# Kernel optimization log

Measured on AMD Instinct MI355X. Metric: run time of the kernel, lower is better.

Reference implementation:

```python
import jax, jax.numpy as jnp
import numpy as np

D_MODEL = 1024
N_HEADS = 16
D_HEAD = D_MODEL // N_HEADS
SCALE = 1.0 / np.sqrt(D_HEAD)


def setup_inputs() -> dict:
    key = jax.random.key(0)
    ks = jax.random.split(key, 5)
    B, S = 2, 2048
    x = jax.random.normal(ks[0], (B, S, D_MODEL), dtype=jnp.float32)
    # torch F.linear weights have shape (d_out, d_in); kaiming-uniform-ish init
    bound = 1.0 / np.sqrt(D_MODEL)
    Wq = jax.random.uniform(ks[1], (D_MODEL, D_MODEL), jnp.float32, -bound, bound)
    Wk = jax.random.uniform(ks[2], (D_MODEL, D_MODEL), jnp.float32, -bound, bound)
    Wv = jax.random.uniform(ks[3], (D_MODEL, D_MODEL), jnp.float32, -bound, bound)
    Wo = jax.random.uniform(ks[4], (D_MODEL, D_MODEL), jnp.float32, -bound, bound)
    return {"x": x, "Wq": Wq, "Wk": Wk, "Wv": Wv, "Wo": Wo}


def reference(x, Wq, Wk, Wv, Wo):
    B, S, _ = x.shape
    # F.linear(x, W) = x @ W.T; reshape to [B, H, S, Dh]
    def proj(W):
        return (x @ W.T).reshape(B, S, N_HEADS, D_HEAD).transpose(0, 2, 1, 3)
    Q, K, V = proj(Wq), proj(Wk), proj(Wv)
    # scores [B, H, S, S]
    attn = jnp.einsum('bhqd,bhkd->bhqk', Q, K) * SCALE
    causal = jnp.tril(jnp.ones((S, S), dtype=bool))
    attn = jnp.where(causal, attn, -jnp.inf)
    attn = jax.nn.softmax(attn, axis=-1)
    out = jnp.einsum('bhqk,bhkd->bhqd', attn, V)
    out = out.transpose(0, 2, 1, 3).reshape(B, S, D_MODEL)
    return out @ Wo.T
```

## Files before the change

### kernel.cpp

```cpp
#include <hip/hip_runtime.h>


typedef __attribute__((ext_vector_type(8))) short short8;
typedef __attribute__((ext_vector_type(4))) float f32x4;
typedef __attribute__((ext_vector_type(4))) _Float16 half4;

#if __has_builtin(__builtin_amdgcn_exp2f)
#define EXP2F(x) __builtin_amdgcn_exp2f(x)
#else
#define EXP2F(x) exp2f(x)
#endif

__device__ __forceinline__ unsigned short f2bf(float f) {
  unsigned int x = __float_as_uint(f);
  x += 0x7fffu + ((x >> 16) & 1u);
  return (unsigned short)(x >> 16);
}

__device__ __forceinline__ void gload16(const void* g, void* l) {
  __builtin_amdgcn_global_load_lds(
      (const __attribute__((address_space(1))) void*)g,
      (__attribute__((address_space(3))) void*)l, 16, 0, 0);
}

__device__ __forceinline__ int swz64(int row, int sc) {
  return row * 64 + ((((sc >> 3) ^ (row & 7)) << 3) | (sc & 7));
}

__device__ __forceinline__ int swzG(int row, int chunk) {
  return row * 32 + (((chunk ^ ((row >> 1) & 3)) << 3));
}

__global__ void cast_kernel(const float* __restrict__ x, const float* __restrict__ wq,
                            const float* __restrict__ wk, const float* __restrict__ wv,
                            const float* __restrict__ wo,
                            unsigned short* __restrict__ xb, unsigned short* __restrict__ wqb,
                            unsigned short* __restrict__ wkb, unsigned short* __restrict__ wvb,
                            unsigned short* __restrict__ wob) {
  int id = blockIdx.x;
  const float* in; unsigned short* out; int blk; float sc = 1.f;
  if (id < 4096) { in = x; out = xb; blk = id; }
  else {
    int wsel = (id - 4096) >> 10;
    blk = (id - 4096) & 1023;
    switch (wsel) {
      case 0: in = wq; out = wqb; sc = 0.18033688011112042f; break;
      case 1: in = wk; out = wkb; break;
      case 2: in = wv; out = wvb; break;
      default: in = wo; out = wob; break;
    }
  }
  int i = blk * 256 + threadIdx.x;
  float4 v = ((const float4*)in)[i];
  union { unsigned short u[4]; uint2 p; } o;
  o.u[0] = f2bf(v.x * sc); o.u[1] = f2bf(v.y * sc);
  o.u[2] = f2bf(v.z * sc); o.u[3] = f2bf(v.w * sc);
  ((uint2*)out)[i] = o.p;
}

#define GK 1024

__global__ __launch_bounds__(256) void gemm_qkv_kernel(
    const unsigned short* __restrict__ X,
    const unsigned short* __restrict__ Wq,
    const unsigned short* __restrict__ Wk,
    const unsigned short* __restrict__ Wv,
    unsigned short* __restrict__ Qo,
    unsigned short* __restrict__ Ko,
    _Float16* __restrict__ Vt) {
  __shared__ unsigned short As[2][128 * 32];
  __shared__ unsigned short Bs[2][128 * 32];
  int mb = blockIdx.x;
  int nbT = blockIdx.y;
  int sel = nbT >> 3, nb = nbT & 7;
  const unsigned short* W = sel == 0 ? Wq : (sel == 1 ? Wk : Wv);

  int tid = threadIdx.x;
  int w = tid >> 6, l = tid & 63, quad = l >> 4, lo = l & 15;
  int wm = (w >> 1) * 64, wn = (w & 1) * 64;

  int srow = tid >> 2;
  int slc = (tid & 3) ^ ((srow >> 1) & 3);
  int srow2 = (256 + tid) >> 2;
  int slc2 = (tid & 3) ^ ((srow2 >> 1) & 3);

  f32x4 acc[4][4];
#pragma unroll
  for (int i = 0; i < 4; i++)
#pragma unroll
    for (int j = 0; j < 4; j++) acc[i][j] = (f32x4){0.f, 0.f, 0.f, 0.f};

  gload16(X + (size_t)(mb * 128 + srow) * GK + slc * 8, (char*)As[0] + tid * 16);
  gload16(W + (size_t)(nb * 128 + srow) * GK + slc * 8, (char*)Bs[0] + tid * 16);
  gload16(X + (size_t)(mb * 128 + srow2) * GK + slc2 * 8, (char*)As[0] + (256 + tid) * 16);
  gload16(W + (size_t)(nb * 128 + srow2) * GK + slc2 * 8, (char*)Bs[0] + (256 + tid) * 16);

  for (int kt = 0; kt < 32; kt++) {
    __syncthreads();
    if (kt + 1 < 32) {
      int nb_ = (kt + 1) & 1, k0 = (kt + 1) * 32;
      gload16(X + (size_t)(mb * 128 + srow) * GK + k0 + slc * 8, (char*)As[nb_] + tid * 16);
      gload16(W + (size_t)(nb * 128 + srow) * GK + k0 + slc * 8, (char*)Bs[nb_] + tid * 16);
      gload16(X + (size_t)(mb * 128 + srow2) * GK + k0 + slc2 * 8,
              (char*)As[nb_] + (256 + tid) * 16);
      gload16(W + (size_t)(nb * 128 + srow2) * GK + k0 + slc2 * 8,
              (char*)Bs[nb_] + (256 + tid) * 16);
    }
    const unsigned short* as = As[kt & 1];
    const unsigned short* bs = Bs[kt & 1];
    short8 a[4], b[4];
#pragma unroll
    for (int mi = 0; mi < 4; mi++)
      a[mi] = *(const short8*)&as[swzG(wm + mi * 16 + lo, quad)];
#pragma unroll
    for (int ni = 0; ni < 4; ni++)
      b[ni] = *(const short8*)&bs[swzG(wn + ni * 16 + lo, quad)];
#pragma unroll
    for (int mi = 0; mi < 4; mi++)
#pragma unroll
      for (int ni = 0; ni < 4; ni++)
        acc[mi][ni] = __builtin_amdgcn_mfma_f32_16x16x32_bf16(a[mi], b[ni],
                                                              acc[mi][ni], 0, 0, 0);
  }
  if (sel == 2) {
#pragma unroll
    for (int mi = 0; mi < 4; mi++)
#pragma unroll
      for (int ni = 0; ni < 4; ni++) {
        int row0 = mb * 128 + wm + mi * 16 + quad * 4;
        int col = nb * 128 + wn + ni * 16 + lo;
        int bb = row0 >> 11, ss = row0 & 2047;
        int hh = col >> 6, dd = col & 63;
        half4 v;
#pragma unroll
        for (int r = 0; r < 4; r++) v[r] = (_Float16)acc[mi][ni][r];
        *(half4*)&Vt[((size_t)((bb * 16 + hh) * 64 + dd)) * 2048 + ss] = v;
      }
  } else {
    unsigned short* C = sel == 0 ? Qo : Ko;
#pragma unroll
    for (int mi = 0; mi < 4; mi++)
#pragma unroll
      for (int ni = 0; ni < 4; ni++)
#pragma unroll
        for (int r = 0; r < 4; r++) {
          int row = mb * 128 + wm + mi * 16 + quad * 4 + r;
          int col = nb * 128 + wn + ni * 16 + lo;
          C[(size_t)row * 1024 + col] = f2bf(acc[mi][ni][r]);
        }
  }
}

__global__ __launch_bounds__(256) void gemm_out_kernel(
    const unsigned short* __restrict__ A,
    const unsigned short* __restrict__ W,
    float* __restrict__ C) {
  __shared__ unsigned short As[2][128 * 32];
  __shared__ unsigned short Bs[2][64 * 32];
  int mb = blockIdx.x, nb = blockIdx.y;
  int tid = threadIdx.x;
  int w = tid >> 6, l = tid & 63, quad = l >> 4, lo = l & 15;
  int wm = w * 32;

  int srow = tid >> 2;
  int slc = (tid & 3) ^ ((srow >> 1) & 3);
  int srow2 = (256 + tid) >> 2;
  int slc2 = (tid & 3) ^ ((srow2 >> 1) & 3);

  f32x4 acc[2][4];
#pragma unroll
  for (int i = 0; i < 2; i++)
#pragma unroll
    for (int j = 0; j < 4; j++) acc[i][j] = (f32x4){0.f, 0.f, 0.f, 0.f};

  gload16(A + (size_t)(mb * 128 + srow) * GK + slc * 8, (char*)As[0] + tid * 16);
  gload16(A + (size_t)(mb * 128 + srow2) * GK + slc2 * 8, (char*)As[0] + (256 + tid) * 16);
  gload16(W + (size_t)(nb * 64 + srow) * GK + slc * 8, (char*)Bs[0] + tid * 16);

  for (int kt = 0; kt < 32; kt++) {
    __syncthreads();
    if (kt + 1 < 32) {
      int nb_ = (kt + 1) & 1, k0 = (kt + 1) * 32;
      gload16(A + (size_t)(mb * 128 + srow) * GK + k0 + slc * 8, (char*)As[nb_] + tid * 16);
      gload16(A + (size_t)(mb * 128 + srow2) * GK + k0 + slc2 * 8,
              (char*)As[nb_] + (256 + tid) * 16);
      gload16(W + (size_t)(nb * 64 + srow) * GK + k0 + slc * 8, (char*)Bs[nb_] + tid * 16);
    }
    const unsigned short* as = As[kt & 1];
    const unsigned short* bs = Bs[kt & 1];
    short8 a[2], b[4];
#pragma unroll
    for (int mi = 0; mi < 2; mi++)
      a[mi] = *(const short8*)&as[swzG(wm + mi * 16 + lo, quad)];
#pragma unroll
    for (int ni = 0; ni < 4; ni++)
      b[ni] = *(const short8*)&bs[swzG(ni * 16 + lo, quad)];
#pragma unroll
    for (int mi = 0; mi < 2; mi++)
#pragma unroll
      for (int ni = 0; ni < 4; ni++)
        acc[mi][ni] = __builtin_amdgcn_mfma_f32_16x16x32_bf16(a[mi], b[ni],
                                                              acc[mi][ni], 0, 0, 0);
  }
#pragma unroll
  for (int mi = 0; mi < 2; mi++)
#pragma unroll
    for (int ni = 0; ni < 4; ni++)
#pragma unroll
      for (int r = 0; r < 4; r++) {
        int row = mb * 128 + wm + mi * 16 + quad * 4 + r;
        int col = nb * 64 + ni * 16 + lo;
        C[(size_t)row * 1024 + col] = acc[mi][ni][r];
      }
}

__global__ __launch_bounds__(256, 4) void attn_kernel(
    const unsigned short* __restrict__ Q,
    const unsigned short* __restrict__ K,
    const _Float16* __restrict__ Vt,
    unsigned short* __restrict__ O) {
  const int S = 2048, DM = 1024;
  __shared__ unsigned short Ks[2][64 * 64];
  __shared__ _Float16 Vts[2][64 * 64];

  int id = blockIdx.x;
  int bh = id & 31;
  int qt = 31 - (id >> 5);
  int b = bh >> 4, h = bh & 15;
  size_t base = (size_t)b * S * DM + h * 64;
  size_t baseVt = (size_t)(bh * 64) * S;

  int tid = threadIdx.x;
  int w = tid >> 6, lane = tid & 63, quad = lane >> 4, lo = lane & 15;
  int qrow0 = qt * 64 + w * 16;
  const half4 ones = {(_Float16)1.f, (_Float16)1.f, (_Float16)1.f, (_Float16)1.f};

  short8 qf[2];
#pragma unroll
  for (int d = 0; d < 2; d++)
    qf[d] = *(const short8*)(Q + base + (size_t)(qrow0 + lo) * DM + d * 32 + quad * 8);

#pragma unroll
  for (int j = 0; j < 2; j++) {
    int s_ = j * 256 + tid;
    int row = s_ >> 3, lc = (s_ & 7) ^ (row & 7);
    gload16(K + base + (size_t)row * DM + lc * 8, (char*)Ks[0] + s_ * 16);
    gload16(Vt + baseVt + (size_t)row * S + lc * 8, (char*)Vts[0] + s_ * 16);
  }

  f32x4 oacc[4], lacc;
  lacc = (f32x4){0.f, 0.f, 0.f, 0.f};
#pragma unroll
  for (int ni = 0; ni < 4; ni++) oacc[ni] = (f32x4){0.f, 0.f, 0.f, 0.f};

  int tend = qt + 1;
  for (int t = 0; t < tend; t++) {
    __syncthreads();
    if (t + 1 < tend) {
      int tb = (t + 1) & 1;
#pragma unroll
      for (int j = 0; j < 2; j++) {
        int s_ = j * 256 + tid;
        int row = s_ >> 3, lc = (s_ & 7) ^ (row & 7);
        gload16(K + base + (size_t)((t + 1) * 64 + row) * DM + lc * 8,
                (char*)Ks[tb] + s_ * 16);
        gload16(Vt + baseVt + (size_t)row * S + (t + 1) * 64 + lc * 8,
                (char*)Vts[tb] + s_ * 16);
      }
    }
    const unsigned short* ks = Ks[t & 1];
    const _Float16* vs = Vts[t & 1];

    f32x4 st[4];
#pragma unroll
    for (int kvt = 0; kvt < 4; kvt++) st[kvt] = (f32x4){0.f, 0.f, 0.f, 0.f};
#pragma unroll
    for (int kvt = 0; kvt < 4; kvt++)
#pragma unroll
      for (int d = 0; d < 2; d++) {
        short8 kf = *(const short8*)&ks[swz64(kvt * 16 + lo, d * 32 + quad * 8)];
        st[kvt] = __builtin_amdgcn_mfma_f32_16x16x32_bf16(kf, qf[d], st[kvt], 0, 0, 0);
      }

    if (t == tend - 1) {
      int qg = qrow0 + lo;
#pragma unroll
      for (int kvt = 0; kvt < 4; kvt++)
#pragma unroll
        for (int r = 0; r < 4; r++) {
          int kv = t * 64 + kvt * 16 + quad * 4 + r;
          if (kv > qg) st[kvt][r] = -1e30f;
        }
    }

    half4 pf[4];
#pragma unroll
    for (int kvt = 0; kvt < 4; kvt++) {
      half4 p4;
#pragma unroll
      for (int r = 0; r < 4; r++) p4[r] = (_Float16)EXP2F(st[kvt][r]);
      pf[kvt] = p4;
    }

#pragma unroll
    for (int kvt = 0; kvt < 4; kvt++) {
#pragma unroll
      for (int ni = 0; ni < 4; ni++) {
        half4 vf = *(const half4*)&vs[swz64(ni * 16 + lo, kvt * 16 + quad * 4)];
        oacc[ni] = __builtin_amdgcn_mfma_f32_16x16x16f16(pf[kvt], vf, oacc[ni], 0, 0, 0);
      }
      lacc = __builtin_amdgcn_mfma_f32_16x16x16f16(pf[kvt], ones, lacc, 0, 0, 0);
    }
  }

  float inv[4];
#pragma unroll
  for (int r = 0; r < 4; r++) inv[r] = 1.0f / lacc[r];
#pragma unroll
  for (int ni = 0; ni < 4; ni++)
#pragma unroll
    for (int r = 0; r < 4; r++) {
      int qg = qrow0 + quad * 4 + r;
      O[base + (size_t)qg * DM + ni * 16 + lo] = f2bf(oacc[ni][r] * inv[r]);
    }
}

extern "C" void kernel_launch(void* const* d_in, const int* in_sizes, int n_in,
                              void* d_out, int out_size, void* d_ws, size_t ws_size,
                              hipStream_t stream) {
  const float* x  = (const float*)d_in[0];
  const float* Wq = (const float*)d_in[1];
  const float* Wk = (const float*)d_in[2];
  const float* Wv = (const float*)d_in[3];
  const float* Wo = (const float*)d_in[4];
  float* out = (float*)d_out;
  char* ws = (char*)d_ws;

  unsigned short* Xb  = (unsigned short*)(ws);
  unsigned short* Wqb = (unsigned short*)(ws + (8ll  << 20));
  unsigned short* Wkb = (unsigned short*)(ws + (10ll << 20));
  unsigned short* Wvb = (unsigned short*)(ws + (12ll << 20));
  unsigned short* Wob = (unsigned short*)(ws + (14ll << 20));
  unsigned short* Qb  = (unsigned short*)(ws + (16ll << 20));
  unsigned short* Kb  = (unsigned short*)(ws + (24ll << 20));
  _Float16*       Vt  = (_Float16*)     (ws + (32ll << 20));
  unsigned short* Ob  = (unsigned short*)(ws + (40ll << 20));

  cast_kernel<<<8192, 256, 0, stream>>>(x, Wq, Wk, Wv, Wo, Xb, Wqb, Wkb, Wvb, Wob);
  gemm_qkv_kernel<<<dim3(32, 24), 256, 0, stream>>>(Xb, Wqb, Wkb, Wvb, Qb, Kb, Vt);
  attn_kernel<<<1024, 256, 0, stream>>>(Qb, Kb, Vt, Ob);
  gemm_out_kernel<<<dim3(32, 16), 256, 0, stream>>>(Ob, Wob, out);
}
```

Measured before the change: 178.4 us.

## Triple-buffer GEMM LDS tiles with two-stage-ahead async prefetch

Both projection GEMM kernels move from double to triple LDS buffering. Global-to-LDS loads are issued two k-tiles ahead, and the loop uses explicit s_waitcnt vmcnt plus a raw s_barrier in place of __syncthreads, so only the oldest tile's loads must finish before compute. This aims to hide more global memory latency. The cost is about 50% more shared memory per block, which may lower occupancy, and correctness now depends on the hand-counted vmcnt values.

```diff
diff --git a/kernel.cpp b/kernel.cpp
--- a/kernel.cpp
+++ b/kernel.cpp
@@ -68,8 +68,8 @@
     unsigned short* __restrict__ Qo,
     unsigned short* __restrict__ Ko,
     _Float16* __restrict__ Vt) {
-  __shared__ unsigned short As[2][128 * 32];
-  __shared__ unsigned short Bs[2][128 * 32];
+  __shared__ unsigned short As[3][128 * 32];
+  __shared__ unsigned short Bs[3][128 * 32];
   int mb = blockIdx.x;
   int nbT = blockIdx.y;
   int sel = nbT >> 3, nb = nbT & 7;
@@ -84,30 +84,42 @@
   int srow2 = (256 + tid) >> 2;
   int slc2 = (tid & 3) ^ ((srow2 >> 1) & 3);
 
+  const unsigned short* Xa = X + (size_t)(mb * 128 + srow) * GK + slc * 8;
+  const unsigned short* Wa = W + (size_t)(nb * 128 + srow) * GK + slc * 8;
+  const unsigned short* Xa2 = X + (size_t)(mb * 128 + srow2) * GK + slc2 * 8;
+  const unsigned short* Wa2 = W + (size_t)(nb * 128 + srow2) * GK + slc2 * 8;
+
   f32x4 acc[4][4];
 #pragma unroll
   for (int i = 0; i < 4; i++)
 #pragma unroll
-    for (int j = 0; j < 4; j++) acc[i][j] = (f32x4){0.f, 0.f, 0.f, 0.f};
-
-  gload16(X + (size_t)(mb * 128 + srow) * GK + slc * 8, (char*)As[0] + tid * 16);
-  gload16(W + (size_t)(nb * 128 + srow) * GK + slc * 8, (char*)Bs[0] + tid * 16);
-  gload16(X + (size_t)(mb * 128 + srow2) * GK + slc2 * 8, (char*)As[0] + (256 + tid) * 16);
-  gload16(W + (size_t)(nb * 128 + srow2) * GK + slc2 * 8, (char*)Bs[0] + (256 + tid) * 16);
+    for (int jj = 0; jj < 4; jj++) acc[i][jj] = (f32x4){0.f, 0.f, 0.f, 0.f};
+
+#pragma unroll
+  for (int p = 0; p < 2; p++) {
+    gload16(Xa + p * 32, (char*)As[p] + tid * 16);
+    gload16(Wa + p * 32, (char*)Bs[p] + tid * 16);
+    gload16(Xa2 + p * 32, (char*)As[p] + (256 + tid) * 16);
+    gload16(Wa2 + p * 32, (char*)Bs[p] + (256 + tid) * 16);
+  }
 
   for (int kt = 0; kt < 32; kt++) {
-    __syncthreads();
-    if (kt + 1 < 32) {
-      int nb_ = (kt + 1) & 1, k0 = (kt + 1) * 32;
-      gload16(X + (size_t)(mb * 128 + srow) * GK + k0 + slc * 8, (char*)As[nb_] + tid * 16);
-      gload16(W + (size_t)(nb * 128 + srow) * GK + k0 + slc * 8, (char*)Bs[nb_] + tid * 16);
-      gload16(X + (size_t)(mb * 128 + srow2) * GK + k0 + slc2 * 8,
-              (char*)As[nb_] + (256 + tid) * 16);
-      gload16(W + (size_t)(nb * 128 + srow2) * GK + k0 + slc2 * 8,
-              (char*)Bs[nb_] + (256 + tid) * 16);
-    }
-    const unsigned short* as = As[kt & 1];
-    const unsigned short* bs = Bs[kt & 1];
+    if (kt < 31) {
+      asm volatile("s_waitcnt vmcnt(4)" ::: "memory");
+    } else {
+      asm volatile("s_waitcnt vmcnt(0)" ::: "memory");
+    }
+    __builtin_amdgcn_s_barrier();
+    asm volatile("" ::: "memory");
+    if (kt + 2 < 32) {
+      int bi = (kt + 2) % 3, k0 = (kt + 2) * 32;
+      gload16(Xa + k0, (char*)As[bi] + tid * 16);
+      gload16(Wa + k0, (char*)Bs[bi] + tid * 16);
+      gload16(Xa2 + k0, (char*)As[bi] + (256 + tid) * 16);
+      gload16(Wa2 + k0, (char*)Bs[bi] + (256 + tid) * 16);
+    }
+    const unsigned short* as = As[kt % 3];
+    const unsigned short* bs = Bs[kt % 3];
     short8 a[4], b[4];
 #pragma unroll
     for (int mi = 0; mi < 4; mi++)
@@ -155,8 +167,8 @@
     const unsigned short* __restrict__ A,
     const unsigned short* __restrict__ W,
     float* __restrict__ C) {
-  __shared__ unsigned short As[2][128 * 32];
-  __shared__ unsigned short Bs[2][64 * 32];
+  __shared__ unsigned short As[3][128 * 32];
+  __shared__ unsigned short Bs[3][64 * 32];
   int mb = blockIdx.x, nb = blockIdx.y;
   int tid = threadIdx.x;
   int w = tid >> 6, l = tid & 63, quad = l >> 4, lo = l & 15;
@@ -167,27 +179,39 @@
   int srow2 = (256 + tid) >> 2;
   int slc2 = (tid & 3) ^ ((srow2 >> 1) & 3);
 
+  const unsigned short* Aa = A + (size_t)(mb * 128 + srow) * GK + slc * 8;
+  const unsigned short* Aa2 = A + (size_t)(mb * 128 + srow2) * GK + slc2 * 8;
+  const unsigned short* Wa = W + (size_t)(nb * 64 + srow) * GK + slc * 8;
+
   f32x4 acc[2][4];
 #pragma unroll
   for (int i = 0; i < 2; i++)
 #pragma unroll
-    for (int j = 0; j < 4; j++) acc[i][j] = (f32x4){0.f, 0.f, 0.f, 0.f};
-
-  gload16(A + (size_t)(mb * 128 + srow) * GK + slc * 8, (char*)As[0] + tid * 16);
-  gload16(A + (size_t)(mb * 128 + srow2) * GK + slc2 * 8, (char*)As[0] + (256 + tid) * 16);
-  gload16(W + (size_t)(nb * 64 + srow) * GK + slc * 8, (char*)Bs[0] + tid * 16);
+    for (int jj = 0; jj < 4; jj++) acc[i][jj] = (f32x4){0.f, 0.f, 0.f, 0.f};
+
+#pragma unroll
+  for (int p = 0; p < 2; p++) {
+    gload16(Aa + p * 32, (char*)As[p] + tid * 16);
+    gload16(Aa2 + p * 32, (char*)As[p] + (256 + tid) * 16);
+    gload16(Wa + p * 32, (char*)Bs[p] + tid * 16);
+  }
 
   for (int kt = 0; kt < 32; kt++) {
-    __syncthreads();
-    if (kt + 1 < 32) {
-      int nb_ = (kt + 1) & 1, k0 = (kt + 1) * 32;
-      gload16(A + (size_t)(mb * 128 + srow) * GK + k0 + slc * 8, (char*)As[nb_] + tid * 16);
-      gload16(A + (size_t)(mb * 128 + srow2) * GK + k0 + slc2 * 8,
-              (char*)As[nb_] + (256 + tid) * 16);
-      gload16(W + (size_t)(nb * 64 + srow) * GK + k0 + slc * 8, (char*)Bs[nb_] + tid * 16);
-    }
-    const unsigned short* as = As[kt & 1];
-    const unsigned short* bs = Bs[kt & 1];
+    if (kt < 31) {
+      asm volatile("s_waitcnt vmcnt(3)" ::: "memory");
+    } else {
+      asm volatile("s_waitcnt vmcnt(0)" ::: "memory");
+    }
+    __builtin_amdgcn_s_barrier();
+    asm volatile("" ::: "memory");
+    if (kt + 2 < 32) {
+      int bi = (kt + 2) % 3, k0 = (kt + 2) * 32;
+      gload16(Aa + k0, (char*)As[bi] + tid * 16);
+      gload16(Aa2 + k0, (char*)As[bi] + (256 + tid) * 16);
+      gload16(Wa + k0, (char*)Bs[bi] + tid * 16);
+    }
+    const unsigned short* as = As[kt % 3];
+    const unsigned short* bs = Bs[kt % 3];
     short8 a[2], b[4];
 #pragma unroll
     for (int mi = 0; mi < 2; mi++)
@@ -241,8 +265,8 @@
     qf[d] = *(const short8*)(Q + base + (size_t)(qrow0 + lo) * DM + d * 32 + quad * 8);
 
 #pragma unroll
-  for (int j = 0; j < 2; j++) {
-    int s_ = j * 256 + tid;
+  for (int jj = 0; jj < 2; jj++) {
+    int s_ = jj * 256 + tid;
     int row = s_ >> 3, lc = (s_ & 7) ^ (row & 7);
     gload16(K + base + (size_t)row * DM + lc * 8, (char*)Ks[0] + s_ * 16);
     gload16(Vt + baseVt + (size_t)row * S + lc * 8, (char*)Vts[0] + s_ * 16);
@@ -259,8 +283,8 @@
     if (t + 1 < tend) {
       int tb = (t + 1) & 1;
 #pragma unroll
-      for (int j = 0; j < 2; j++) {
-        int s_ = j * 256 + tid;
+      for (int jj = 0; jj < 2; jj++) {
+        int s_ = jj * 256 + tid;
         int row = s_ >> 3, lc = (s_ & 7) ^ (row & 7);
         gload16(K + base + (size_t)((t + 1) * 64 + row) * DM + lc * 8,
                 (char*)Ks[tb] + s_ * 16);
```

Result: no change. 178.2 us (-0.1%).
